# Kernel tuning notes

Measured on AMD Instinct MI355X. Metric: run time of the kernel, lower is better.

The kernel has to match this reference:

```python
import jax, jax.numpy as jnp
import numpy as np

N = 100000
E = 3200000
HEADS = 4
DH = 16  # per-head dim
IN = 300
OUT2 = 32
SLOPE = 0.2  # PyG GATConv leaky_relu negative slope


def setup_inputs() -> dict:
    key = jax.random.key(0)
    ks = jax.random.split(key, 10)
    x = jax.random.normal(ks[0], (N, IN), dtype=jnp.float32)
    edge_index = jax.random.randint(ks[1], (2, E), 0, N, dtype=jnp.int64)
    sec_order_edge_index = jax.random.randint(ks[2], (2, E), 0, N, dtype=jnp.int64)
    # GATConv(300, 16, heads=4) params
    W1 = jax.random.normal(ks[3], (IN, HEADS * DH), dtype=jnp.float32) * (1.0 / np.sqrt(IN))
    att_src = jax.random.normal(ks[4], (HEADS, DH), dtype=jnp.float32) * 0.1
    att_dst = jax.random.normal(ks[5], (HEADS, DH), dtype=jnp.float32) * 0.1
    b1 = jnp.zeros((HEADS * DH,), dtype=jnp.float32)
    # GCNConv(64, 32) params
    W2 = jax.random.normal(ks[6], (HEADS * DH, OUT2), dtype=jnp.float32) * (1.0 / np.sqrt(HEADS * DH))
    b2 = jnp.zeros((OUT2,), dtype=jnp.float32)
    return {"x": x, "W1": W1, "att_src": att_src, "att_dst": att_dst, "b1": b1,
            "W2": W2, "b2": b2, "edge_index": edge_index,
            "sec_order_edge_index": sec_order_edge_index}


def _add_self_loops(edge_index, n):
    loop = jnp.arange(n, dtype=edge_index.dtype)
    src = jnp.concatenate([edge_index[0], loop])
    dst = jnp.concatenate([edge_index[1], loop])
    return src, dst


def _gat(x, W1, att_src, att_dst, b1, edge_index):
    n = x.shape[0]
    src, dst = _add_self_loops(edge_index, n)
    h = (x @ W1).reshape(n, HEADS, DH)                    # [N,H,D]
    a_s = jnp.einsum('nhd,hd->nh', h, att_src)            # [N,H]
    a_d = jnp.einsum('nhd,hd->nh', h, att_dst)
    e = jax.nn.leaky_relu(a_s[src] + a_d[dst], SLOPE)     # [Et,H]
    # segment softmax over edges grouped by destination node
    m = jax.ops.segment_max(e, dst, num_segments=n)       # [N,H]
    ex = jnp.exp(e - m[dst])
    denom = jax.ops.segment_sum(ex, dst, num_segments=n)  # [N,H] (>0: self-loops)
    alpha = ex / denom[dst]                               # [Et,H]
    out = jax.ops.segment_sum(h[src] * alpha[:, :, None], dst, num_segments=n)
    return out.reshape(n, HEADS * DH) + b1


def _gcn(x, W2, b2, edge_index):
    n = x.shape[0]
    src, dst = _add_self_loops(edge_index, n)
    deg = jax.ops.segment_sum(jnp.ones_like(dst, dtype=x.dtype), dst, num_segments=n)
    dinv = jnp.where(deg > 0, jax.lax.rsqrt(deg), 0.0)
    norm = dinv[src] * dinv[dst]                          # [Et]
    h = x @ W2                                            # [N,32]
    out = jax.ops.segment_sum(h[src] * norm[:, None], dst, num_segments=n)
    return out + b2


def reference(x, W1, att_src, att_dst, b1, W2, b2, edge_index, sec_order_edge_index):
    x1 = jax.nn.relu(_gat(x, W1, att_src, att_dst, b1, edge_index))
    # F.dropout with training=False is identity (eval mode)
    return _gcn(x1, W2, b2, sec_order_edge_index)
```

## Files before the change

kernel.cpp:

```cpp
#include <hip/hip_runtime.h>
#include <hip/hip_bf16.h>

#define N_NODES 100000
#define N_EDGES 3200000
#define TOT_E   (N_EDGES + N_NODES)
#define HEADS   4
#define DH      16
#define IN_F    300
#define HID     64
#define OUT2    32
#define SLOPE   0.2f
#define NBK     256
#define GSZ     391
#define EBLK    4096
#define NBA     ((TOT_E + EBLK - 1) / EBLK)

#define G1B_ROWS 64
#define G1B_KT   20
#define G1B_NT   15
#define G1B_XP   76

__global__ __launch_bounds__(64, 2) void k_gemm1(const float* __restrict__ x,
                                                 const float* __restrict__ W1,
                                                 float* __restrict__ h) {
    __shared__ __align__(16) float xT[G1B_KT][G1B_XP];
    __shared__ __align__(16) float wl[2][G1B_KT * HID];
    const int t = threadIdx.x;
    const int tc = t & 7, tr = t >> 3;
    const int c0 = tc * 8, r0 = tr * 8;
    const int row0 = blockIdx.x * G1B_ROWS;

    int rj[5], qj[5];
    const float* xp[5];
#pragma unroll
    for (int j = 0; j < 5; j++) {
        int c = j * 64 + t;
        int r = c / 5;
        rj[j] = r;
        qj[j] = c - r * 5;
        int gr = row0 + r;
        gr = (gr < N_NODES) ? gr : (N_NODES - 1);
        xp[j] = x + (size_t)gr * IN_F + qj[j] * 4;
    }

    float acc[8][8];
#pragma unroll
    for (int i = 0; i < 8; i++)
#pragma unroll
        for (int j = 0; j < 8; j++) acc[i][j] = 0.f;

    float4 xr[5];
#pragma unroll
    for (int j = 0; j < 5; j++) xr[j] = *(const float4*)(xp[j]);
#pragma unroll
    for (int m = 0; m < 5; m++)
        __builtin_amdgcn_global_load_lds(
            (const __attribute__((address_space(1))) unsigned int*)(W1 + m * 256 + t * 4),
            (__attribute__((address_space(3))) unsigned int*)(&wl[0][m * 256]),
            16, 0, 0);

    for (int tt = 0; tt < G1B_NT; ++tt) {
#pragma unroll
        for (int j = 0; j < 5; j++) {
            int r = rj[j], kq = qj[j] * 4;
            xT[kq + 0][r] = xr[j].x;
            xT[kq + 1][r] = xr[j].y;
            xT[kq + 2][r] = xr[j].z;
            xT[kq + 3][r] = xr[j].w;
        }
        asm volatile("s_waitcnt vmcnt(0)" ::: "memory");
        if (tt + 1 < G1B_NT) {
            const int kt = (tt + 1) * G1B_KT;
#pragma unroll
            for (int j = 0; j < 5; j++) xr[j] = *(const float4*)(xp[j] + kt);
            const float* wsrc = W1 + kt * HID;
            float* wdst = wl[(tt + 1) & 1];
#pragma unroll
            for (int m = 0; m < 5; m++)
                __builtin_amdgcn_global_load_lds(
                    (const __attribute__((address_space(1))) unsigned int*)(wsrc + m * 256 + t * 4),
                    (__attribute__((address_space(3))) unsigned int*)(wdst + m * 256),
                    16, 0, 0);
        }
        const float* wb = wl[tt & 1];
#pragma unroll 4
        for (int k = 0; k < G1B_KT; k++) {
            float4 xa = *(const float4*)&xT[k][r0];
            float4 xb = *(const float4*)&xT[k][r0 + 4];
            float4 wa = *(const float4*)&wb[k * HID + c0];
            float4 wc = *(const float4*)&wb[k * HID + c0 + 4];
            float xv[8] = {xa.x, xa.y, xa.z, xa.w, xb.x, xb.y, xb.z, xb.w};
            float wv[8] = {wa.x, wa.y, wa.z, wa.w, wc.x, wc.y, wc.z, wc.w};
#pragma unroll
            for (int i = 0; i < 8; i++)
#pragma unroll
                for (int j = 0; j < 8; j++)
                    acc[i][j] += xv[i] * wv[j];
        }
    }

#pragma unroll
    for (int i = 0; i < 8; i++) {
        int gr = row0 + r0 + i;
        if (gr < N_NODES) {
            *(float4*)&h[(size_t)gr * HID + c0] =
                make_float4(acc[i][0], acc[i][1], acc[i][2], acc[i][3]);
            *(float4*)&h[(size_t)gr * HID + c0 + 4] =
                make_float4(acc[i][4], acc[i][5], acc[i][6], acc[i][7]);
        }
    }
}

__global__ void k_scores(const float* __restrict__ h,
                         const float* __restrict__ att_src,
                         const float* __restrict__ att_dst,
                         float* __restrict__ as_ad) {
    int tid = blockIdx.x * blockDim.x + threadIdx.x;
    if (tid >= N_NODES * HEADS) return;
    int n = tid >> 2, hd = tid & 3;
    const float* hp = &h[(size_t)n * HID + hd * DH];
    float s = 0.f, d = 0.f;
#pragma unroll
    for (int k = 0; k < DH; k++) {
        float v = hp[k];
        s += v * att_src[hd * DH + k];
        d += v * att_dst[hd * DH + k];
    }
    as_ad[n * 8 + hd] = s;
    as_ad[n * 8 + 4 + hd] = d;
}

__global__ __launch_bounds__(512) void k_chist(const int* __restrict__ ei1,
                                               const int* __restrict__ ei2,
                                               int* __restrict__ ccnt) {
    __shared__ int hist[NBK];
    int b = blockIdx.x; const int* ei; int* cc;
    if (b < NBA) { ei = ei1; cc = ccnt; }
    else         { ei = ei2; cc = ccnt + NBK; b -= NBA; }
    int t = threadIdx.x;
    if (t < NBK) hist[t] = 0;
    __syncthreads();
    int e0 = b * EBLK;
#pragma unroll
    for (int i = 0; i < 8; i++) {
        int e = e0 + i * 512 + t;
        if (e < TOT_E) {
            int dst = (e < N_EDGES) ? ei[N_EDGES + e] : (e - N_EDGES);
            atomicAdd(&hist[(unsigned int)dst / GSZ], 1);
        }
    }
    __syncthreads();
    if (t < NBK) { int v = hist[t]; if (v) atomicAdd(&cc[t], v); }
}

__global__ __launch_bounds__(512) void k_cscan(const int* __restrict__ ccnt,
                                               int* __restrict__ crp,
                                               int* __restrict__ ccur) {
    __shared__ int sc[512];
    int t = threadIdx.x;
    int idx = t & (NBK - 1);
    int own = ccnt[t];
    sc[t] = own;
    __syncthreads();
    for (int off = 1; off < NBK; off <<= 1) {
        int v = (idx >= off) ? sc[t - off] : 0;
        __syncthreads();
        sc[t] += v;
        __syncthreads();
    }
    int ex = sc[t] - own;
    crp[t] = ex; ccur[t] = ex;
}

__global__ __launch_bounds__(512) void k_binA(const int* __restrict__ ei1,
                                              const int* __restrict__ ei2,
                                              int* __restrict__ ccur,
                                              unsigned int* __restrict__ tmp) {
    __shared__ int hist[NBK];
    __shared__ int base[NBK];
    int b = blockIdx.x; const int* ei; int loff;
    if (b < NBA) { ei = ei1; loff = 0; }
    else         { ei = ei2; loff = 1; b -= NBA; }
    int t = threadIdx.x;
    if (t < NBK) hist[t] = 0;
    __syncthreads();
    unsigned int pk[8]; int cb[8], rk[8];
    int e0 = b * EBLK;
#pragma unroll
    for (int i = 0; i < 8; i++) {
        int e = e0 + i * 512 + t;
        cb[i] = -1;
        if (e < TOT_E) {
            int src, dst;
            if (e < N_EDGES) { src = ei[e]; dst = ei[N_EDGES + e]; }
            else             { src = e - N_EDGES; dst = src; }
            unsigned int c   = (unsigned int)dst / GSZ;
            unsigned int dlo = (unsigned int)dst - c * GSZ;
            cb[i] = (int)c;
            pk[i] = (dlo << 17) | (unsigned int)src;
            rk[i] = atomicAdd(&hist[c], 1);
        }
    }
    __syncthreads();
    if (t < NBK) {
        int v = hist[t];
        base[t] = v ? atomicAdd(&ccur[loff * NBK + t], v) : 0;
    }
    __syncthreads();
    unsigned int* tp = tmp + (size_t)loff * TOT_E;
#pragma unroll
    for (int i = 0; i < 8; i++)
        if (cb[i] >= 0) tp[base[cb[i]] + rk[i]] = pk[i];
}

__global__ __launch_bounds__(256) void k_binB(const unsigned int* __restrict__ tmp,
                                              const int* __restrict__ crp,
                                              int* __restrict__ rowptr,
                                              int* __restrict__ srcs,
                                              float* __restrict__ dinv) {
    __shared__ int cnt[GSZ + 1];
    __shared__ int sc[512];
    __shared__ int cur[GSZ + 1];
    int blk = blockIdx.x;
    int l = blk >> 8, b = blk & 255;
    int t = threadIdx.x;
    int nbeg = b * GSZ;
    int ncnt = min(GSZ, N_NODES - nbeg);
    const int* crpl = crp + l * NBK;
    int ebeg = crpl[b];
    int eend = (b < NBK - 1) ? crpl[b + 1] : TOT_E;
    const unsigned int* tp = tmp + (size_t)l * TOT_E;
    for (int i = t; i < GSZ + 1; i += 256) cnt[i] = 0;
    __syncthreads();
    for (int e = ebeg + t; e < eend; e += 256)
        atomicAdd(&cnt[tp[e] >> 17], 1);
    __syncthreads();
    int t2 = t + 256;
    sc[t]  = (t  < ncnt) ? cnt[t]  : 0;
    sc[t2] = (t2 < ncnt) ? cnt[t2] : 0;
    __syncthreads();
    for (int off = 1; off < 512; off <<= 1) {
        int v0 = (t  >= off) ? sc[t  - off] : 0;
        int v1 = (t2 >= off) ? sc[t2 - off] : 0;
        __syncthreads();
        sc[t] += v0; sc[t2] += v1;
        __syncthreads();
    }
    for (int i = t; i < ncnt; i += 256) {
        int c = cnt[i];
        int gpos = ebeg + sc[i] - c;
        rowptr[l * N_NODES + nbeg + i] = gpos;
        cur[i] = gpos;
        if (l == 1) dinv[nbeg + i] = rsqrtf((float)c);
    }
    __syncthreads();
    int* so = srcs + (size_t)l * TOT_E;
    for (int e = ebeg + t; e < eend; e += 256) {
        unsigned int p = tp[e];
        int pos = atomicAdd(&cur[p >> 17], 1);
        so[pos] = (int)(p & 0x1FFFF);
    }
}

__global__ __launch_bounds__(256) void k_gat(const float* __restrict__ h,
                                             const float* __restrict__ as_ad,
                                             const int* __restrict__ rowptr,
                                             const int* __restrict__ srcs,
                                             const float* __restrict__ b1,
                                             float* __restrict__ x1) {
    int w = (blockIdx.x * 256 + threadIdx.x) >> 6;
    if (w >= N_NODES) return;
    int lane = threadIdx.x & 63;
    int eidx = lane >> 4;
    int cl = lane & 15;
    int hd = cl >> 2;
    int c0 = cl * 4;
    float ad = as_ad[w * 8 + 4 + hd];
    int beg = rowptr[w];
    int end = (w == N_NODES - 1) ? TOT_E : rowptr[w + 1];
    float l = 0.f;
    float ax = 0.f, ay = 0.f, az = 0.f, aw = 0.f;
#pragma unroll 2
    for (int j = beg; j < end; j += 4) {
        int je = j + eidx;
        int s = srcs[min(je, end - 1)];
        float4 h4 = *(const float4*)&h[(size_t)s * HID + c0];
        float e = as_ad[s * 8 + hd] + ad;
        e = fminf((e > 0.f) ? e : SLOPE * e, 60.f);
        float p = (je < end) ? __expf(e) : 0.f;
        l += p;
        ax += p * h4.x; ay += p * h4.y; az += p * h4.z; aw += p * h4.w;
    }
    l  += __shfl_xor(l, 16, 64);  l  += __shfl_xor(l, 32, 64);
    ax += __shfl_xor(ax, 16, 64); ax += __shfl_xor(ax, 32, 64);
    ay += __shfl_xor(ay, 16, 64); ay += __shfl_xor(ay, 32, 64);
    az += __shfl_xor(az, 16, 64); az += __shfl_xor(az, 32, 64);
    aw += __shfl_xor(aw, 16, 64); aw += __shfl_xor(aw, 32, 64);
    if (eidx == 0) {
        float4 bv = *(const float4*)&b1[c0];
        float rl = 1.f / l;
        float4 o = make_float4(fmaxf(ax * rl + bv.x, 0.f),
                               fmaxf(ay * rl + bv.y, 0.f),
                               fmaxf(az * rl + bv.z, 0.f),
                               fmaxf(aw * rl + bv.w, 0.f));
        *(float4*)&x1[(size_t)w * HID + c0] = o;
    }
}

__global__ __launch_bounds__(256) void k_gemm2(const float* __restrict__ x1,
                                               const float* __restrict__ W2,
                                               const float* __restrict__ dinv,
                                               float* __restrict__ h2s) {
    __shared__ float wl[HID * OUT2];
    __shared__ float xl[8][HID];
    int t = threadIdx.x;
    for (int i = t; i < HID * OUT2; i += 256) wl[i] = W2[i];
    int row0 = blockIdx.x * 8;
    for (int i = t; i < 8 * HID; i += 256) {
        int rr = i >> 6, kk = i & 63;
        int gr = row0 + rr;
        xl[rr][kk] = (gr < N_NODES) ? x1[(size_t)gr * HID + kk] : 0.f;
    }
    __syncthreads();
    int r = t >> 5, c = t & 31;
    float acc = 0.f;
#pragma unroll 8
    for (int k = 0; k < HID; k++) acc += xl[r][k] * wl[k * OUT2 + c];
    int gr = row0 + r;
    if (gr < N_NODES) h2s[(size_t)gr * OUT2 + c] = acc * dinv[gr];
}

__global__ __launch_bounds__(256) void k_gcn(const float* __restrict__ h2s,
                                             const float* __restrict__ dinv,
                                             const int* __restrict__ rowptr,
                                             const int* __restrict__ srcs,
                                             const float* __restrict__ b2,
                                             float* __restrict__ out) {
    int w = (blockIdx.x * 256 + threadIdx.x) >> 6;
    if (w >= N_NODES) return;
    int lane = threadIdx.x & 63;
    int eidx = lane >> 3;
    int cq = lane & 7;
    int c0 = cq * 4;
    int beg = rowptr[w];
    int end = (w == N_NODES - 1) ? TOT_E : rowptr[w + 1];
    float ax = 0.f, ay = 0.f, az = 0.f, aw = 0.f;
#pragma unroll 2
    for (int j = beg; j < end; j += 8) {
        int je = j + eidx;
        int s = srcs[min(je, end - 1)];
        float4 h4 = *(const float4*)&h2s[(size_t)s * OUT2 + c0];
        if (je < end) { ax += h4.x; ay += h4.y; az += h4.z; aw += h4.w; }
    }
    ax += __shfl_xor(ax, 8, 64); ax += __shfl_xor(ax, 16, 64); ax += __shfl_xor(ax, 32, 64);
    ay += __shfl_xor(ay, 8, 64); ay += __shfl_xor(ay, 16, 64); ay += __shfl_xor(ay, 32, 64);
    az += __shfl_xor(az, 8, 64); az += __shfl_xor(az, 16, 64); az += __shfl_xor(az, 32, 64);
    aw += __shfl_xor(aw, 8, 64); aw += __shfl_xor(aw, 16, 64); aw += __shfl_xor(aw, 32, 64);
    if (eidx == 0) {
        float dv = dinv[w];
        float4 bv = *(const float4*)&b2[c0];
        float4 o = make_float4(ax * dv + bv.x, ay * dv + bv.y,
                               az * dv + bv.z, aw * dv + bv.w);
        *(float4*)&out[(size_t)w * OUT2 + c0] = o;
    }
}

static inline size_t align_up(size_t v, size_t a) { return (v + a - 1) & ~(a - 1); }

extern "C" void kernel_launch(void* const* d_in, const int* in_sizes, int n_in,
                              void* d_out, int out_size, void* d_ws, size_t ws_size,
                              hipStream_t stream) {
    const float* x       = (const float*)d_in[0];
    const float* W1      = (const float*)d_in[1];
    const float* att_src = (const float*)d_in[2];
    const float* att_dst = (const float*)d_in[3];
    const float* b1      = (const float*)d_in[4];
    const float* W2      = (const float*)d_in[5];
    const float* b2      = (const float*)d_in[6];
    const int*   ei1     = (const int*)d_in[7];
    const int*   ei2     = (const int*)d_in[8];
    float* out = (float*)d_out;

    char* p = (char*)d_ws;
    size_t off = 0;
    auto carve = [&](size_t bytes) { void* q = p + off; off = align_up(off + bytes, 256); return q; };
    float* h      = (float*)carve((size_t)N_NODES * HID * 4);
    float* x1     = (float*)carve((size_t)N_NODES * HID * 4);
    float* h2s    = (float*)carve((size_t)N_NODES * OUT2 * 4);
    float* as_ad  = (float*)carve((size_t)N_NODES * 8 * 4);
    float* dinv   = (float*)carve((size_t)N_NODES * 4);
    int* rowptr   = (int*)carve((size_t)2 * N_NODES * 4);
    int* srcs     = (int*)carve((size_t)2 * TOT_E * 4);
    int* ccnt     = (int*)carve((size_t)2 * NBK * 4);
    int* crp      = (int*)carve((size_t)2 * NBK * 4);
    int* ccur     = (int*)carve((size_t)2 * NBK * 4);
    unsigned int* tmp = (unsigned int*)x1;
    (void)ws_size; (void)in_sizes; (void)n_in; (void)out_size;

    hipMemsetAsync(ccnt, 0, (size_t)2 * NBK * 4, stream);

    k_gemm1<<<(N_NODES + G1B_ROWS - 1) / G1B_ROWS, 64, 0, stream>>>(x, W1, h);
    k_scores<<<(N_NODES * HEADS + 255) / 256, 256, 0, stream>>>(h, att_src, att_dst, as_ad);

    k_chist<<<2 * NBA, 512, 0, stream>>>(ei1, ei2, ccnt);
    k_cscan<<<1, 512, 0, stream>>>(ccnt, crp, ccur);
    k_binA<<<2 * NBA, 512, 0, stream>>>(ei1, ei2, ccur, tmp);
    k_binB<<<2 * NBK, 256, 0, stream>>>(tmp, crp, rowptr, srcs, dinv);

    k_gat<<<N_NODES / 4, 256, 0, stream>>>(h, as_ad, rowptr, srcs, b1, x1);

    k_gemm2<<<N_NODES / 8, 256, 0, stream>>>(x1, W2, dinv, h2s);

    k_gcn<<<N_NODES / 4, 256, 0, stream>>>(h2s, dinv, rowptr + N_NODES, srcs + TOT_E, b2, out);
}
```

Before: 631.2 us.

## Store GAT hidden features in fp16 and gather eight edges per wave

The first GEMM now writes the projected node features as fp16, which halves the bytes moved by the per-edge random gathers in the GAT aggregation. The GAT kernel is restructured so each lane loads 8 halves (16 bytes) and a wave covers 8 edges per iteration instead of 4, with a three-step shuffle reduction. Attention scores are computed from the fp16 values. This costs some precision in the hidden features and scores, plus extra shuffle work per node.

```diff
diff --git a/kernel.cpp b/kernel.cpp
--- a/kernel.cpp
+++ b/kernel.cpp
@@ -1,5 +1,5 @@
 #include <hip/hip_runtime.h>
-#include <hip/hip_bf16.h>
+#include <hip/hip_fp16.h>
 
 #define N_NODES 100000
 #define N_EDGES 3200000
@@ -22,7 +22,7 @@
 
 __global__ __launch_bounds__(64, 2) void k_gemm1(const float* __restrict__ x,
                                                  const float* __restrict__ W1,
-                                                 float* __restrict__ h) {
+                                                 __half* __restrict__ h16) {
     __shared__ __align__(16) float xT[G1B_KT][G1B_XP];
     __shared__ __align__(16) float wl[2][G1B_KT * HID];
     const int t = threadIdx.x;
@@ -103,28 +103,33 @@
     for (int i = 0; i < 8; i++) {
         int gr = row0 + r0 + i;
         if (gr < N_NODES) {
-            *(float4*)&h[(size_t)gr * HID + c0] =
-                make_float4(acc[i][0], acc[i][1], acc[i][2], acc[i][3]);
-            *(float4*)&h[(size_t)gr * HID + c0 + 4] =
-                make_float4(acc[i][4], acc[i][5], acc[i][6], acc[i][7]);
-        }
-    }
-}
-
-__global__ void k_scores(const float* __restrict__ h,
+            __half2 q[4];
+            q[0] = __floats2half2_rn(acc[i][0], acc[i][1]);
+            q[1] = __floats2half2_rn(acc[i][2], acc[i][3]);
+            q[2] = __floats2half2_rn(acc[i][4], acc[i][5]);
+            q[3] = __floats2half2_rn(acc[i][6], acc[i][7]);
+            *(float4*)&h16[(size_t)gr * HID + c0] = *(float4*)q;
+        }
+    }
+}
+
+__global__ void k_scores(const __half* __restrict__ h16,
                          const float* __restrict__ att_src,
                          const float* __restrict__ att_dst,
                          float* __restrict__ as_ad) {
     int tid = blockIdx.x * blockDim.x + threadIdx.x;
     if (tid >= N_NODES * HEADS) return;
     int n = tid >> 2, hd = tid & 3;
-    const float* hp = &h[(size_t)n * HID + hd * DH];
+    const __half* hp = &h16[(size_t)n * HID + hd * DH];
+    __half2 hv[8];
+    *(float4*)&hv[0] = *(const float4*)hp;
+    *(float4*)&hv[4] = *(const float4*)(hp + 8);
     float s = 0.f, d = 0.f;
 #pragma unroll
-    for (int k = 0; k < DH; k++) {
-        float v = hp[k];
-        s += v * att_src[hd * DH + k];
-        d += v * att_dst[hd * DH + k];
+    for (int k = 0; k < 8; k++) {
+        float2 f = __half22float2(hv[k]);
+        s += f.x * att_src[hd * DH + 2 * k] + f.y * att_src[hd * DH + 2 * k + 1];
+        d += f.x * att_dst[hd * DH + 2 * k] + f.y * att_dst[hd * DH + 2 * k + 1];
     }
     as_ad[n * 8 + hd] = s;
     as_ad[n * 8 + 4 + hd] = d;
@@ -262,7 +267,7 @@
     }
 }
 
-__global__ __launch_bounds__(256) void k_gat(const float* __restrict__ h,
+__global__ __launch_bounds__(256) void k_gat(const __half* __restrict__ h16,
                                              const float* __restrict__ as_ad,
                                              const int* __restrict__ rowptr,
                                              const int* __restrict__ srcs,
@@ -271,39 +276,56 @@
     int w = (blockIdx.x * 256 + threadIdx.x) >> 6;
     if (w >= N_NODES) return;
     int lane = threadIdx.x & 63;
-    int eidx = lane >> 4;
-    int cl = lane & 15;
-    int hd = cl >> 2;
-    int c0 = cl * 4;
+    int eidx = lane >> 3;
+    int cl = lane & 7;
+    int hd = cl >> 1;
+    int c0 = cl * 8;
     float ad = as_ad[w * 8 + 4 + hd];
     int beg = rowptr[w];
     int end = (w == N_NODES - 1) ? TOT_E : rowptr[w + 1];
     float l = 0.f;
-    float ax = 0.f, ay = 0.f, az = 0.f, aw = 0.f;
+    float a0 = 0.f, a1 = 0.f, a2 = 0.f, a3 = 0.f;
+    float a4 = 0.f, a5 = 0.f, a6 = 0.f, a7 = 0.f;
 #pragma unroll 2
-    for (int j = beg; j < end; j += 4) {
+    for (int j = beg; j < end; j += 8) {
         int je = j + eidx;
         int s = srcs[min(je, end - 1)];
-        float4 h4 = *(const float4*)&h[(size_t)s * HID + c0];
+        float4 raw = *(const float4*)&h16[(size_t)s * HID + c0];
         float e = as_ad[s * 8 + hd] + ad;
-        e = fminf((e > 0.f) ? e : SLOPE * e, 60.f);
+        e = fminf(fmaxf(e, SLOPE * e), 60.f);
         float p = (je < end) ? __expf(e) : 0.f;
         l += p;
-        ax += p * h4.x; ay += p * h4.y; az += p * h4.z; aw += p * h4.w;
-    }
-    l  += __shfl_xor(l, 16, 64);  l  += __shfl_xor(l, 32, 64);
-    ax += __shfl_xor(ax, 16, 64); ax += __shfl_xor(ax, 32, 64);
-    ay += __shfl_xor(ay, 16, 64); ay += __shfl_xor(ay, 32, 64);
-    az += __shfl_xor(az, 16, 64); az += __shfl_xor(az, 32, 64);
-    aw += __shfl_xor(aw, 16, 64); aw += __shfl_xor(aw, 32, 64);
+        const __half2* hv = (const __half2*)&raw;
+        float2 f0 = __half22float2(hv[0]);
+        float2 f1 = __half22float2(hv[1]);
+        float2 f2 = __half22float2(hv[2]);
+        float2 f3 = __half22float2(hv[3]);
+        a0 += p * f0.x; a1 += p * f0.y; a2 += p * f1.x; a3 += p * f1.y;
+        a4 += p * f2.x; a5 += p * f2.y; a6 += p * f3.x; a7 += p * f3.y;
+    }
+    l  += __shfl_xor(l, 8, 64);  l  += __shfl_xor(l, 16, 64);  l  += __shfl_xor(l, 32, 64);
+    a0 += __shfl_xor(a0, 8, 64); a0 += __shfl_xor(a0, 16, 64); a0 += __shfl_xor(a0, 32, 64);
+    a1 += __shfl_xor(a1, 8, 64); a1 += __shfl_xor(a1, 16, 64); a1 += __shfl_xor(a1, 32, 64);
+    a2 += __shfl_xor(a2, 8, 64); a2 += __shfl_xor(a2, 16, 64); a2 += __shfl_xor(a2, 32, 64);
+    a3 += __shfl_xor(a3, 8, 64); a3 += __shfl_xor(a3, 16, 64); a3 += __shfl_xor(a3, 32, 64);
+    a4 += __shfl_xor(a4, 8, 64); a4 += __shfl_xor(a4, 16, 64); a4 += __shfl_xor(a4, 32, 64);
+    a5 += __shfl_xor(a5, 8, 64); a5 += __shfl_xor(a5, 16, 64); a5 += __shfl_xor(a5, 32, 64);
+    a6 += __shfl_xor(a6, 8, 64); a6 += __shfl_xor(a6, 16, 64); a6 += __shfl_xor(a6, 32, 64);
+    a7 += __shfl_xor(a7, 8, 64); a7 += __shfl_xor(a7, 16, 64); a7 += __shfl_xor(a7, 32, 64);
     if (eidx == 0) {
-        float4 bv = *(const float4*)&b1[c0];
         float rl = 1.f / l;
-        float4 o = make_float4(fmaxf(ax * rl + bv.x, 0.f),
-                               fmaxf(ay * rl + bv.y, 0.f),
-                               fmaxf(az * rl + bv.z, 0.f),
-                               fmaxf(aw * rl + bv.w, 0.f));
-        *(float4*)&x1[(size_t)w * HID + c0] = o;
+        float4 b0 = *(const float4*)&b1[c0];
+        float4 b4 = *(const float4*)&b1[c0 + 4];
+        float4 o0 = make_float4(fmaxf(a0 * rl + b0.x, 0.f),
+                                fmaxf(a1 * rl + b0.y, 0.f),
+                                fmaxf(a2 * rl + b0.z, 0.f),
+                                fmaxf(a3 * rl + b0.w, 0.f));
+        float4 o4 = make_float4(fmaxf(a4 * rl + b4.x, 0.f),
+                                fmaxf(a5 * rl + b4.y, 0.f),
+                                fmaxf(a6 * rl + b4.z, 0.f),
+                                fmaxf(a7 * rl + b4.w, 0.f));
+        *(float4*)&x1[(size_t)w * HID + c0] = o0;
+        *(float4*)&x1[(size_t)w * HID + c0 + 4] = o4;
     }
 }
 
@@ -384,7 +406,7 @@
     char* p = (char*)d_ws;
     size_t off = 0;
     auto carve = [&](size_t bytes) { void* q = p + off; off = align_up(off + bytes, 256); return q; };
-    float* h      = (float*)carve((size_t)N_NODES * HID * 4);
+    __half* h16   = (__half*)carve((size_t)N_NODES * HID * 2);
     float* x1     = (float*)carve((size_t)N_NODES * HID * 4);
     float* h2s    = (float*)carve((size_t)N_NODES * OUT2 * 4);
     float* as_ad  = (float*)carve((size_t)N_NODES * 8 * 4);
@@ -399,15 +421,15 @@
 
     hipMemsetAsync(ccnt, 0, (size_t)2 * NBK * 4, stream);
 
-    k_gemm1<<<(N_NODES + G1B_ROWS - 1) / G1B_ROWS, 64, 0, stream>>>(x, W1, h);
-    k_scores<<<(N_NODES * HEADS + 255) / 256, 256, 0, stream>>>(h, att_src, att_dst, as_ad);
+    k_gemm1<<<(N_NODES + G1B_ROWS - 1) / G1B_ROWS, 64, 0, stream>>>(x, W1, h16);
+    k_scores<<<(N_NODES * HEADS + 255) / 256, 256, 0, stream>>>(h16, att_src, att_dst, as_ad);
 
     k_chist<<<2 * NBA, 512, 0, stream>>>(ei1, ei2, ccnt);
     k_cscan<<<1, 512, 0, stream>>>(ccnt, crp, ccur);
     k_binA<<<2 * NBA, 512, 0, stream>>>(ei1, ei2, ccur, tmp);
     k_binB<<<2 * NBK, 256, 0, stream>>>(tmp, crp, rowptr, srcs, dinv);
 
-    k_gat<<<N_NODES / 4, 256, 0, stream>>>(h, as_ad, rowptr, srcs, b1, x1);
+    k_gat<<<N_NODES / 4, 256, 0, stream>>>(h16, as_ad, rowptr, srcs, b1, x1);
 
     k_gemm2<<<N_NODES / 8, 256, 0, stream>>>(x1, W2, dinv, h2s);
 
```

After: 572.2 us. -9.3%, faster.
